# Kernel tuning notes

Measured on AMD Instinct MI355X. Metric: run time of the kernel, lower is better.

## Reference

```python
import jax, jax.numpy as jnp
import numpy as np

N_USERS = 90000
N_ITEMS = 60000
N = N_USERS + N_ITEMS   # 150000 total nodes
D = 64                  # emb_dim
K = 128                 # n_intents
E = 1600000             # directed edges
L = 3                   # n_layers
EPS = 1e-12


def setup_inputs() -> dict:
    key = jax.random.key(0)
    k0, k1, k2, k3, k4 = jax.random.split(key, 5)
    embeddings = jax.random.normal(k0, (N, D), dtype=jnp.float32) * 0.1
    user_intent = jax.random.normal(k1, (D, K), dtype=jnp.float32) * 0.1
    item_intent = jax.random.normal(k2, (D, K), dtype=jnp.float32) * 0.1
    all_h = jax.random.randint(k3, (E,), 0, N, dtype=jnp.int32)
    all_t = jax.random.randint(k4, (E,), 0, N, dtype=jnp.int32)
    return {"embeddings": embeddings, "user_intent": user_intent,
            "item_intent": item_intent, "all_h": all_h, "all_t": all_t}


def _spmm(vals, h, t, x):
    # y[i] = sum_{e: h[e]==i} vals[e] * x[t[e]]   (sparse adj @ x)
    return jax.ops.segment_sum(vals[:, None] * x[t], h, num_segments=N)


def _sym_norm_values(h, t):
    # G = D^{-1/2} A D^{-1/2} edge values (A has unit edge weights)
    deg = jax.ops.segment_sum(jnp.ones((E,), jnp.float32), h, num_segments=N)
    d_inv = jnp.where(deg > 0, deg ** -0.5, 0.0)
    return d_inv[h] * d_inv[t]


def _adaptive_values(head_emb, tail_emb, h):
    # F.normalize: x / max(||x||, eps)
    hn = head_emb / jnp.maximum(jnp.linalg.norm(head_emb, axis=1, keepdims=True), EPS)
    tn = tail_emb / jnp.maximum(jnp.linalg.norm(tail_emb, axis=1, keepdims=True), EPS)
    edge_alpha = (jnp.sum(hn * tn, axis=1) + 1.0) * 0.5          # [E]
    row_sum = jax.ops.segment_sum(edge_alpha, h, num_segments=N)  # degree scores
    d_inv = jnp.where(row_sum > 0, 1.0 / row_sum, 0.0)           # pow(-1).nan_to_num
    return d_inv[h] * edge_alpha


def reference(embeddings, user_intent, item_intent, all_h, all_t):
    g_vals = _sym_norm_values(all_h, all_t)
    x = embeddings
    acc = x  # sum over all layer embeddings (incl. layer 0)
    for _ in range(L):
        gnn = _spmm(g_vals, all_h, all_t, x)
        u, it = x[:N_USERS], x[N_USERS:]
        u_int = jax.nn.softmax(u @ user_intent, axis=1) @ user_intent.T
        i_int = jax.nn.softmax(it @ item_intent, axis=1) @ item_intent.T
        intl = jnp.concatenate([u_int, i_int], axis=0)            # [N, D]
        gaa_vals = _adaptive_values(gnn[all_h], gnn[all_t], all_h)
        iaa_vals = _adaptive_values(intl[all_h], intl[all_t], all_h)
        gaa = _spmm(gaa_vals, all_h, all_t, x)
        iaa = _spmm(iaa_vals, all_h, all_t, x)
        x = gnn + intl + gaa + iaa + x
        acc = acc + x
    return acc
```

## Files before the change

### kernel.cpp

```cpp
#include <hip/hip_runtime.h>

#define N_USERS 90000
#define N_ITEMS 60000
#define NN      (N_USERS + N_ITEMS)
#define D       64
#define KDIM    128
#define NE      1600000
#define EPSF    1e-12f
#define ROWD    64
#define TU      ((N_USERS + 63) / 64)
#define TI      ((N_ITEMS + 63) / 64)
#define NINT    (TU + TI)
#define RB      ((NN + 3) / 4)


typedef __fp16 h2 __attribute__((ext_vector_type(2)));
typedef float  f2 __attribute__((ext_vector_type(2)));

__device__ inline h2 as_h2(unsigned u) {
    union { unsigned u; h2 h; } v; v.u = u; return v.h;
}
__device__ inline unsigned pkrtz(float a, float b) {
    auto r = __builtin_amdgcn_cvt_pkrtz(a, b);
    union { decltype(r) h; unsigned u; } v; v.h = r; return v.u;
}
__device__ inline f2 dec8lo(unsigned u) {
    return __builtin_amdgcn_cvt_pk_f32_fp8((int)u, false);
}
__device__ inline f2 dec8hi(unsigned u) {
    return __builtin_amdgcn_cvt_pk_f32_fp8((int)u, true);
}
__device__ inline unsigned enc8(float a, float b, float c, float d) {
    int u = __builtin_amdgcn_cvt_pk_fp8_f32(a, b, 0, false);
    u = __builtin_amdgcn_cvt_pk_fp8_f32(c, d, u, true);
    return (unsigned)u;
}


#define EB   ((NE + 255) / 256)
#define IB   ((NN * 16 + 255) / 256)
#define PREG (EB + IB + 64)

__global__ void k_pre(const int* __restrict__ h, int* __restrict__ deg,
                      const float* __restrict__ emb,
                      float* __restrict__ acc, unsigned* __restrict__ pkA,
                      const float* __restrict__ Wu, const float* __restrict__ Wi,
                      float* __restrict__ WtG) {
    int bid = blockIdx.x;
    if (bid < EB) {
        int e = bid * 256 + threadIdx.x;
        if (e < NE) atomicAdd(&deg[h[e]], 1);
    } else if (bid < EB + IB) {
        int i = (bid - EB) * 256 + threadIdx.x;
        if (i >= NN * 16) return;
        float4 v = ((const float4*)emb)[i];
        ((float4*)acc)[i] = v;
        int row = i >> 4, l = i & 15;
        *(uint2*)&pkA[(size_t)row * ROWD + 32 + 2 * l] =
            make_uint2(pkrtz(v.x, v.y), pkrtz(v.z, v.w));
    } else {
        int i = (bid - EB - IB) * 256 + threadIdx.x;
        if (i >= 2 * D * KDIM) return;
        int m = i >> 13, r = i & 8191;
        int k = r >> 6, d = r & 63;
        const float* W = m ? Wi : Wu;
        WtG[m * 8192 + k * 64 + d] = W[d * KDIM + k];
    }
}

__global__ void k_rowoff(const int* __restrict__ deg, int* __restrict__ counter,
                         int* __restrict__ row_off, float* __restrict__ d_inv) {
    int i = blockIdx.x * blockDim.x + threadIdx.x;
    if (i >= NN) return;
    int d = deg[i];
    row_off[i] = atomicAdd(counter, d);
    d_inv[i]   = (d > 0) ? rsqrtf((float)d) : 0.f;
}

__global__ void k_scatter(const int* __restrict__ h, const int* __restrict__ t,
                          const int* __restrict__ row_off, int* __restrict__ row_cur,
                          const float* __restrict__ d_inv,
                          int2* __restrict__ csr) {
    int e = blockIdx.x * blockDim.x + threadIdx.x;
    if (e >= NE) return;
    int hh = h[e], tt = t[e];
    int slot = row_off[hh] + atomicAdd(&row_cur[hh], 1);
    csr[slot] = make_int2(tt, __float_as_int(d_inv[hh] * d_inv[tt]));
}

__global__ __launch_bounds__(256) void k_mid(const int* __restrict__ row_off,
                                             const int* __restrict__ deg,
                                             const int2* __restrict__ csr,
                                             unsigned* __restrict__ pk,
                                             unsigned* __restrict__ intl_h,
                                             const float* __restrict__ Wu,
                                             const float* __restrict__ Wi,
                                             const float* __restrict__ WtG,
                                             float* __restrict__ base_) {
    __shared__ float xs[64 * 68];
    int tid = threadIdx.x;
    int bid = blockIdx.x;

    if (bid < NINT) {
        unsigned* psU = (unsigned*)xs;
        const float* W;
        const float* Wt;
        int bse, count, n0;
        if (bid < TU) {
            W = Wu; Wt = WtG;        bse = 0;       count = N_USERS; n0 = bid * 64;
        } else {
            W = Wi; Wt = WtG + 8192; bse = N_USERS; count = N_ITEMS; n0 = (bid - TU) * 64;
        }

        for (int i = tid; i < 64 * 32; i += 256) {
            int nl = i >> 5, dw = i & 31;
            int n  = n0 + nl;
            unsigned u = (n < count) ? pk[(size_t)(bse + n) * ROWD + 32 + dw] : 0u;
            h2 xv = as_h2(u);
            xs[(2 * dw) * 68 + nl]     = (float)xv.x;
            xs[(2 * dw + 1) * 68 + nl] = (float)xv.y;
        }
        __syncthreads();

        int wv = tid >> 6;
        int la = tid & 63;
        int ag = la >> 4;
        int bg = la & 15;
        int nbase = wv * 16 + ag * 4;

        float acc[4][8];
        #pragma unroll
        for (int i = 0; i < 4; ++i)
            #pragma unroll
            for (int j = 0; j < 8; ++j) acc[i][j] = 0.f;

        #pragma unroll 4
        for (int d = 0; d < 64; ++d) {
            float4 xv = *(const float4*)&xs[d * 68 + nbase];
            float4 wa = *(const float4*)&W[d * KDIM + 4 * bg];
            float4 wb = *(const float4*)&W[d * KDIM + 64 + 4 * bg];
            float xx[4] = {xv.x, xv.y, xv.z, xv.w};
            float wk[8] = {wa.x, wa.y, wa.z, wa.w, wb.x, wb.y, wb.z, wb.w};
            #pragma unroll
            for (int i = 0; i < 4; ++i)
                #pragma unroll
                for (int j = 0; j < 8; ++j)
                    acc[i][j] = fmaf(xx[i], wk[j], acc[i][j]);
        }

        float p[4][8];
        float inv_s[4];
        #pragma unroll
        for (int i = 0; i < 4; ++i) {
            float m = acc[i][0];
            #pragma unroll
            for (int j = 1; j < 8; ++j) m = fmaxf(m, acc[i][j]);
            m = fmaxf(m, __shfl_xor(m, 1));
            m = fmaxf(m, __shfl_xor(m, 2));
            m = fmaxf(m, __shfl_xor(m, 4));
            m = fmaxf(m, __shfl_xor(m, 8));
            float sm = 0.f;
            #pragma unroll
            for (int j = 0; j < 8; ++j) { p[i][j] = __expf(acc[i][j] - m); sm += p[i][j]; }
            sm += __shfl_xor(sm, 1);
            sm += __shfl_xor(sm, 2);
            sm += __shfl_xor(sm, 4);
            sm += __shfl_xor(sm, 8);
            inv_s[i] = 1.f / sm;
        }

        __syncthreads();

        #pragma unroll
        for (int i = 0; i < 4; ++i) {
            float is = inv_s[i];
            #pragma unroll
            for (int j = 0; j < 2; ++j) {
                unsigned u0 = pkrtz(p[i][4 * j + 0] * is, p[i][4 * j + 1] * is);
                unsigned u1 = pkrtz(p[i][4 * j + 2] * is, p[i][4 * j + 3] * is);
                *(uint2*)&psU[(nbase + i) * 66 + 2 * bg + 32 * j] = make_uint2(u0, u1);
            }
        }
        __syncthreads();

        float o[4][4];
        #pragma unroll
        for (int i = 0; i < 4; ++i)
            #pragma unroll
            for (int r = 0; r < 4; ++r) o[i][r] = 0.f;

        int dbase = bg * 4;
        for (int kk = 0; kk < 32; ++kk) {
            uint2 P[4];
            #pragma unroll
            for (int i = 0; i < 4; ++i)
                P[i] = *(const uint2*)&psU[(nbase + i) * 66 + 2 * kk];
            float4 Wv[4];
            #pragma unroll
            for (int c = 0; c < 4; ++c)
                Wv[c] = *(const float4*)&Wt[(4 * kk + c) * 64 + dbase];
            #pragma unroll
            for (int i = 0; i < 4; ++i) {
                h2 pa = as_h2(P[i].x), pb = as_h2(P[i].y);
                float pc[4] = {(float)pa.x, (float)pa.y, (float)pb.x, (float)pb.y};
                #pragma unroll
                for (int c = 0; c < 4; ++c) {
                    o[i][0] = fmaf(pc[c], Wv[c].x, o[i][0]);
                    o[i][1] = fmaf(pc[c], Wv[c].y, o[i][1]);
                    o[i][2] = fmaf(pc[c], Wv[c].z, o[i][2]);
                    o[i][3] = fmaf(pc[c], Wv[c].w, o[i][3]);
                }
            }
        }

        #pragma unroll
        for (int i = 0; i < 4; ++i) {
            int n = n0 + nbase + i;
            float ss = o[i][0]*o[i][0] + o[i][1]*o[i][1] + o[i][2]*o[i][2] + o[i][3]*o[i][3];
            ss += __shfl_xor(ss, 1);
            ss += __shfl_xor(ss, 2);
            ss += __shfl_xor(ss, 4);
            ss += __shfl_xor(ss, 8);
            if (n < count) {
                size_t g = (size_t)(bse + n);
                float invn = 1.0f / fmaxf(sqrtf(ss), EPSF);
                *(uint2*)&intl_h[g * 32 + 2 * bg] =
                    make_uint2(pkrtz(o[i][0], o[i][1]), pkrtz(o[i][2], o[i][3]));
                pk[g * ROWD + 2 * bg + 1] =
                    enc8(o[i][0] * invn, o[i][1] * invn, o[i][2] * invn, o[i][3] * invn);
            }
        }
    } else {
        int wid  = (bid - NINT) * 4 + (tid >> 6);
        int lane = tid & 63;
        if (wid >= NN) return;
        int grp = lane >> 3, l8 = lane & 7;
        int s = row_off[wid], eend = s + deg[wid];
        float a0 = 0.f, a1 = 0.f, a2 = 0.f, a3 = 0.f;
        float a4 = 0.f, a5 = 0.f, a6 = 0.f, a7 = 0.f;
        int e = s;
        int2 c = csr[min(s + grp, eend - 1)];
        for (; e + 7 < eend; e += 8) {
            int2 cn = csr[min(e + 8 + grp, eend - 1)];
            uint4 w = *(const uint4*)&pk[(size_t)c.x * ROWD + 32 + 4 * l8];
            float gv = __int_as_float(c.y);
            h2 x0 = as_h2(w.x), x1 = as_h2(w.y), x2 = as_h2(w.z), x3 = as_h2(w.w);
            a0 = fmaf(gv, (float)x0.x, a0); a1 = fmaf(gv, (float)x0.y, a1);
            a2 = fmaf(gv, (float)x1.x, a2); a3 = fmaf(gv, (float)x1.y, a3);
            a4 = fmaf(gv, (float)x2.x, a4); a5 = fmaf(gv, (float)x2.y, a5);
            a6 = fmaf(gv, (float)x3.x, a6); a7 = fmaf(gv, (float)x3.y, a7);
            c = cn;
        }
        if (e < eend) {
            bool val = e + grp < eend;
            float gv = val ? __int_as_float(c.y) : 0.f;
            uint4 w = *(const uint4*)&pk[(size_t)c.x * ROWD + 32 + 4 * l8];
            h2 x0 = as_h2(w.x), x1 = as_h2(w.y), x2 = as_h2(w.z), x3 = as_h2(w.w);
            a0 = fmaf(gv, (float)x0.x, a0); a1 = fmaf(gv, (float)x0.y, a1);
            a2 = fmaf(gv, (float)x1.x, a2); a3 = fmaf(gv, (float)x1.y, a3);
            a4 = fmaf(gv, (float)x2.x, a4); a5 = fmaf(gv, (float)x2.y, a5);
            a6 = fmaf(gv, (float)x3.x, a6); a7 = fmaf(gv, (float)x3.y, a7);
        }
        #pragma unroll
        for (int m = 8; m <= 32; m <<= 1) {
            a0 += __shfl_xor(a0, m); a1 += __shfl_xor(a1, m);
            a2 += __shfl_xor(a2, m); a3 += __shfl_xor(a3, m);
            a4 += __shfl_xor(a4, m); a5 += __shfl_xor(a5, m);
            a6 += __shfl_xor(a6, m); a7 += __shfl_xor(a7, m);
        }
        float ss = fmaf(a0, a0, fmaf(a1, a1, fmaf(a2, a2, a3 * a3)))
                 + fmaf(a4, a4, fmaf(a5, a5, fmaf(a6, a6, a7 * a7)));
        ss += __shfl_xor(ss, 1); ss += __shfl_xor(ss, 2); ss += __shfl_xor(ss, 4);
        float inv = 1.f / fmaxf(sqrtf(ss), EPSF);
        if (grp == 0) {
            unsigned* pr = pk + (size_t)wid * ROWD;
            pr[4 * l8]     = enc8(a0 * inv, a1 * inv, a2 * inv, a3 * inv);
            pr[4 * l8 + 2] = enc8(a4 * inv, a5 * inv, a6 * inv, a7 * inv);
            uint4 xw = *(const uint4*)&pr[32 + 4 * l8];
            h2 x0 = as_h2(xw.x), x1 = as_h2(xw.y), x2 = as_h2(xw.z), x3 = as_h2(xw.w);
            float4* bp = (float4*)base_ + (size_t)wid * 16 + 2 * l8;
            bp[0] = make_float4(a0 + (float)x0.x, a1 + (float)x0.y,
                                a2 + (float)x1.x, a3 + (float)x1.y);
            bp[1] = make_float4(a4 + (float)x2.x, a5 + (float)x2.y,
                                a6 + (float)x3.x, a7 + (float)x3.y);
        }
    }
}

__global__ __launch_bounds__(256) void k_fused(const int* __restrict__ row_off,
                                               const int* __restrict__ deg,
                                               const int2* __restrict__ csr,
                                               const unsigned* __restrict__ pk,
                                               const unsigned* __restrict__ intl_h,
                                               const float* __restrict__ base_,
                                               unsigned* __restrict__ pknext,
                                               float* __restrict__ acc) {
    int wid  = (blockIdx.x * blockDim.x + threadIdx.x) >> 6;
    int lane = threadIdx.x & 63;
    if (wid >= NN) return;
    int grp = lane >> 4, l16 = lane & 15;

    const unsigned* ph = pk + (size_t)wid * ROWD;
    uint2 hq = *(const uint2*)&ph[2 * l16];
    f2 hgl = dec8lo(hq.x), hgh = dec8hi(hq.x);
    f2 hil = dec8lo(hq.y), hih = dec8hi(hq.y);

    int s = row_off[wid], eend = s + deg[wid];
    float sg = 0.f, si = 0.f;
    float g0 = 0.f, g1 = 0.f, g2 = 0.f, g3 = 0.f;
    float i0 = 0.f, i1 = 0.f, i2 = 0.f, i3 = 0.f;

    int e = s;
    int tA = csr[min(s + grp, eend - 1)].x;
    int tB = csr[min(s + 4 + grp, eend - 1)].x;
    for (; e + 7 < eend; e += 8) {
        int tA2 = csr[min(e + 8 + grp, eend - 1)].x;
        int tB2 = csr[min(e + 12 + grp, eend - 1)].x;
        const unsigned* pA = pk + (size_t)tA * ROWD;
        const unsigned* pB = pk + (size_t)tB * ROWD;
        uint2 qA = *(const uint2*)&pA[2 * l16];
        uint2 wA = *(const uint2*)&pA[32 + 2 * l16];
        uint2 qB = *(const uint2*)&pB[2 * l16];
        uint2 wB = *(const uint2*)&pB[32 + 2 * l16];
        f2 gA01 = dec8lo(qA.x), gA23 = dec8hi(qA.x);
        f2 iA01 = dec8lo(qA.y), iA23 = dec8hi(qA.y);
        f2 gB01 = dec8lo(qB.x), gB23 = dec8hi(qB.x);
        f2 iB01 = dec8lo(qB.y), iB23 = dec8hi(qB.y);
        float pgA = fmaf(hgl.x, gA01.x, fmaf(hgl.y, gA01.y,
                    fmaf(hgh.x, gA23.x, hgh.y * gA23.y)));
        float piA = fmaf(hil.x, iA01.x, fmaf(hil.y, iA01.y,
                    fmaf(hih.x, iA23.x, hih.y * iA23.y)));
        float pgB = fmaf(hgl.x, gB01.x, fmaf(hgl.y, gB01.y,
                    fmaf(hgh.x, gB23.x, hgh.y * gB23.y)));
        float piB = fmaf(hil.x, iB01.x, fmaf(hil.y, iB01.y,
                    fmaf(hih.x, iB23.x, hih.y * iB23.y)));
        #pragma unroll
        for (int m = 1; m <= 8; m <<= 1) {
            pgA += __shfl_xor(pgA, m); piA += __shfl_xor(piA, m);
            pgB += __shfl_xor(pgB, m); piB += __shfl_xor(piB, m);
        }
        float agA = fmaf(pgA, 0.5f, 0.5f), aiA = fmaf(piA, 0.5f, 0.5f);
        float agB = fmaf(pgB, 0.5f, 0.5f), aiB = fmaf(piB, 0.5f, 0.5f);
        sg += agA + agB; si += aiA + aiB;
        h2 xa0 = as_h2(wA.x), xa1 = as_h2(wA.y);
        h2 xb0 = as_h2(wB.x), xb1 = as_h2(wB.y);
        g0 = fmaf(agA, (float)xa0.x, g0); g1 = fmaf(agA, (float)xa0.y, g1);
        g2 = fmaf(agA, (float)xa1.x, g2); g3 = fmaf(agA, (float)xa1.y, g3);
        i0 = fmaf(aiA, (float)xa0.x, i0); i1 = fmaf(aiA, (float)xa0.y, i1);
        i2 = fmaf(aiA, (float)xa1.x, i2); i3 = fmaf(aiA, (float)xa1.y, i3);
        g0 = fmaf(agB, (float)xb0.x, g0); g1 = fmaf(agB, (float)xb0.y, g1);
        g2 = fmaf(agB, (float)xb1.x, g2); g3 = fmaf(agB, (float)xb1.y, g3);
        i0 = fmaf(aiB, (float)xb0.x, i0); i1 = fmaf(aiB, (float)xb0.y, i1);
        i2 = fmaf(aiB, (float)xb1.x, i2); i3 = fmaf(aiB, (float)xb1.y, i3);
        tA = tA2; tB = tB2;
    }
    #pragma unroll
    for (int r = 0; r < 2; ++r) {
        if (e >= eend) break;
        int t = (r == 0) ? tA : tB;
        bool val = e + grp < eend;
        const unsigned* pr = pk + (size_t)t * ROWD;
        uint2 q = *(const uint2*)&pr[2 * l16];
        uint2 w = *(const uint2*)&pr[32 + 2 * l16];
        f2 tg01 = dec8lo(q.x), tg23 = dec8hi(q.x);
        f2 ti01 = dec8lo(q.y), ti23 = dec8hi(q.y);
        float pg = fmaf(hgl.x, tg01.x, fmaf(hgl.y, tg01.y,
                   fmaf(hgh.x, tg23.x, hgh.y * tg23.y)));
        float pi = fmaf(hil.x, ti01.x, fmaf(hil.y, ti01.y,
                   fmaf(hih.x, ti23.x, hih.y * ti23.y)));
        #pragma unroll
        for (int m = 1; m <= 8; m <<= 1) {
            pg += __shfl_xor(pg, m); pi += __shfl_xor(pi, m);
        }
        float ag = fmaf(pg, 0.5f, 0.5f), ai = fmaf(pi, 0.5f, 0.5f);
        if (!val) { ag = 0.f; ai = 0.f; }
        sg += ag; si += ai;
        h2 x0 = as_h2(w.x), x1 = as_h2(w.y);
        g0 = fmaf(ag, (float)x0.x, g0); g1 = fmaf(ag, (float)x0.y, g1);
        g2 = fmaf(ag, (float)x1.x, g2); g3 = fmaf(ag, (float)x1.y, g3);
        i0 = fmaf(ai, (float)x0.x, i0); i1 = fmaf(ai, (float)x0.y, i1);
        i2 = fmaf(ai, (float)x1.x, i2); i3 = fmaf(ai, (float)x1.y, i3);
        e += 4;
    }

    #pragma unroll
    for (int m = 16; m <= 32; m <<= 1) {
        sg += __shfl_xor(sg, m); si += __shfl_xor(si, m);
        g0 += __shfl_xor(g0, m); g1 += __shfl_xor(g1, m);
        g2 += __shfl_xor(g2, m); g3 += __shfl_xor(g3, m);
        i0 += __shfl_xor(i0, m); i1 += __shfl_xor(i1, m);
        i2 += __shfl_xor(i2, m); i3 += __shfl_xor(i3, m);
    }

    if (grp == 0) {
        float invg = sg > 0.f ? 1.f / sg : 0.f;
        float invi = si > 0.f ? 1.f / si : 0.f;
        size_t bidx = (size_t)wid * 16 + l16;
        float4 b = ((const float4*)base_)[bidx];
        uint2 iw = *(const uint2*)&intl_h[(size_t)wid * 32 + 2 * l16];
        h2 il0 = as_h2(iw.x), il1 = as_h2(iw.y);
        float o0 = b.x + (float)il0.x + invg * g0 + invi * i0;
        float o1 = b.y + (float)il0.y + invg * g1 + invi * i1;
        float o2 = b.z + (float)il1.x + invg * g2 + invi * i2;
        float o3 = b.w + (float)il1.y + invg * g3 + invi * i3;
        *(uint2*)&pknext[(size_t)wid * ROWD + 32 + 2 * l16] =
            make_uint2(pkrtz(o0, o1), pkrtz(o2, o3));
        float4 a = ((float4*)acc)[bidx];
        a.x += o0; a.y += o1; a.z += o2; a.w += o3;
        ((float4*)acc)[bidx] = a;
    }
}


extern "C" void kernel_launch(void* const* d_in, const int* in_sizes, int n_in,
                              void* d_out, int out_size, void* d_ws, size_t ws_size,
                              hipStream_t stream) {
    const float* emb   = (const float*)d_in[0];
    const float* Wu    = (const float*)d_in[1];
    const float* Wi    = (const float*)d_in[2];
    const int*   all_h = (const int*)d_in[3];
    const int*   all_t = (const int*)d_in[4];
    float*       acc   = (float*)d_out;

    char*  bp  = (char*)d_ws;
    size_t off = 0;
    auto take = [&](size_t bytes) -> char* {
        char* r = bp + off;
        off = (off + bytes + 255) & ~(size_t)255;
        return r;
    };
    int*      deg     = (int*)     take((size_t)NN * 4);
    int*      row_off = (int*)     take((size_t)NN * 4);
    int*      row_cur = (int*)     take((size_t)NN * 4);
    int*      counter = (int*)     take(256);
    float*    d_inv   = (float*)   take((size_t)NN * 4);
    int2*     csr     = (int2*)    take((size_t)NE * 8);
    unsigned* pkA     = (unsigned*)take((size_t)NN * ROWD * 4);
    unsigned* pkB     = (unsigned*)take((size_t)NN * ROWD * 4);
    unsigned* intl_h  = (unsigned*)take((size_t)NN * 32 * 4);
    float*    base_   = (float*)   take((size_t)NN * D * 4);
    float*    WtG     = (float*)   take((size_t)2 * D * KDIM * 4);
    (void)ws_size; (void)in_sizes; (void)n_in; (void)out_size;

    hipMemsetAsync(deg, 0, (size_t)NN * 4, stream);
    hipMemsetAsync(row_cur, 0, (size_t)NN * 4, stream);
    hipMemsetAsync(counter, 0, 256, stream);

    const int NBK = (NN + 255) / 256;
    k_pre<<<PREG, 256, 0, stream>>>(all_h, deg, emb, acc, pkA, Wu, Wi, WtG);
    k_rowoff<<<NBK, 256, 0, stream>>>(deg, counter, row_off, d_inv);
    k_scatter<<<EB, 256, 0, stream>>>(all_h, all_t, row_off, row_cur, d_inv, csr);

    unsigned* cur = pkA;
    unsigned* nxt = pkB;
    for (int l = 0; l < 3; ++l) {
        k_mid<<<NINT + RB, 256, 0, stream>>>(row_off, deg, csr, cur, intl_h,
                                             Wu, Wi, WtG, base_);
        k_fused<<<RB, 256, 0, stream>>>(row_off, deg, csr, cur, intl_h,
                                        base_, nxt, acc);
        unsigned* tmp = cur; cur = nxt; nxt = tmp;
    }
}
```

Before: 910.3 us.

## Compute intent softmax matmuls with fp16 MFMA and pre-packed weight fragments

Replaces the scalar FMA loops for the two intent matmuls (x@W and softmax@W^T) in k_mid with 16x16x32 fp16 MFMA instructions. The weights are pre-packed once in k_pre into per-lane fragment layouts, and the softmax probabilities pass through swizzled LDS to feed the second MFMA. This removes the LDS transpose staging and the fp32 FMA work. In exchange, the weights and probabilities now go through fp16 inputs, and the output write uses lane shuffles and partially masked stores.

New measurement: 792.0 us. -13.0%, faster.

```diff
diff --git a/kernel.cpp b/kernel.cpp
--- a/kernel.cpp
+++ b/kernel.cpp
@@ -15,10 +15,15 @@
 
 
 typedef __fp16 h2 __attribute__((ext_vector_type(2)));
+typedef __fp16 h8 __attribute__((ext_vector_type(8)));
 typedef float  f2 __attribute__((ext_vector_type(2)));
+typedef float  f4v __attribute__((ext_vector_type(4)));
 
 __device__ inline h2 as_h2(unsigned u) {
     union { unsigned u; h2 h; } v; v.u = u; return v.h;
+}
+__device__ inline h8 as_h8(uint4 u) {
+    union { uint4 u; h8 h; } v; v.u = u; return v.h;
 }
 __device__ inline unsigned pkrtz(float a, float b) {
     auto r = __builtin_amdgcn_cvt_pkrtz(a, b);
@@ -39,13 +44,13 @@
 
 #define EB   ((NE + 255) / 256)
 #define IB   ((NN * 16 + 255) / 256)
-#define PREG (EB + IB + 64)
+#define PREG (EB + IB + 16)
 
 __global__ void k_pre(const int* __restrict__ h, int* __restrict__ deg,
                       const float* __restrict__ emb,
                       float* __restrict__ acc, unsigned* __restrict__ pkA,
                       const float* __restrict__ Wu, const float* __restrict__ Wi,
-                      float* __restrict__ WtG) {
+                      uint4* __restrict__ WfA, uint4* __restrict__ Wf2) {
     int bid = blockIdx.x;
     if (bid < EB) {
         int e = bid * 256 + threadIdx.x;
@@ -60,11 +65,28 @@
             make_uint2(pkrtz(v.x, v.y), pkrtz(v.z, v.w));
     } else {
         int i = (bid - EB - IB) * 256 + threadIdx.x;
-        if (i >= 2 * D * KDIM) return;
-        int m = i >> 13, r = i & 8191;
-        int k = r >> 6, d = r & 63;
-        const float* W = m ? Wi : Wu;
-        WtG[m * 8192 + k * 64 + d] = W[d * KDIM + k];
+        if (i >= 4096) return;
+        int ph  = i >> 11;
+        int r   = i & 2047;
+        int mat = r >> 10;
+        int rr  = r & 1023;
+        const float* W = mat ? Wi : Wu;
+        union { __fp16 hh[8]; uint4 u; } pkt;
+        if (!ph) {
+            int nt = rr >> 7, ks = (rr >> 6) & 1, lane = rr & 63;
+            int q = lane >> 4, c = lane & 15;
+            #pragma unroll
+            for (int j = 0; j < 8; ++j)
+                pkt.hh[j] = (__fp16)W[(32 * ks + 8 * q + j) * KDIM + nt * 16 + c];
+            WfA[((mat * 8 + nt) * 2 + ks) * 64 + lane] = pkt.u;
+        } else {
+            int nt = rr >> 8, ks = (rr >> 6) & 3, lane = rr & 63;
+            int q = lane >> 4, c = lane & 15;
+            #pragma unroll
+            for (int j = 0; j < 8; ++j)
+                pkt.hh[j] = (__fp16)W[(nt * 16 + c) * KDIM + 32 * ks + 8 * q + j];
+            Wf2[((mat * 4 + nt) * 4 + ks) * 64 + lane] = pkt.u;
+        }
     }
 }
 
@@ -93,141 +115,115 @@
                                              const int2* __restrict__ csr,
                                              unsigned* __restrict__ pk,
                                              unsigned* __restrict__ intl_h,
-                                             const float* __restrict__ Wu,
-                                             const float* __restrict__ Wi,
-                                             const float* __restrict__ WtG,
+                                             const uint4* __restrict__ WfA,
+                                             const uint4* __restrict__ Wf2,
                                              float* __restrict__ base_) {
-    __shared__ float xs[64 * 68];
+    __shared__ unsigned Plds[4096];
     int tid = threadIdx.x;
     int bid = blockIdx.x;
 
     if (bid < NINT) {
-        unsigned* psU = (unsigned*)xs;
-        const float* W;
-        const float* Wt;
-        int bse, count, n0;
-        if (bid < TU) {
-            W = Wu; Wt = WtG;        bse = 0;       count = N_USERS; n0 = bid * 64;
-        } else {
-            W = Wi; Wt = WtG + 8192; bse = N_USERS; count = N_ITEMS; n0 = (bid - TU) * 64;
-        }
-
-        for (int i = tid; i < 64 * 32; i += 256) {
-            int nl = i >> 5, dw = i & 31;
-            int n  = n0 + nl;
-            unsigned u = (n < count) ? pk[(size_t)(bse + n) * ROWD + 32 + dw] : 0u;
-            h2 xv = as_h2(u);
-            xs[(2 * dw) * 68 + nl]     = (float)xv.x;
-            xs[(2 * dw + 1) * 68 + nl] = (float)xv.y;
-        }
-        __syncthreads();
-
-        int wv = tid >> 6;
-        int la = tid & 63;
-        int ag = la >> 4;
-        int bg = la & 15;
-        int nbase = wv * 16 + ag * 4;
-
-        float acc[4][8];
-        #pragma unroll
-        for (int i = 0; i < 4; ++i)
-            #pragma unroll
-            for (int j = 0; j < 8; ++j) acc[i][j] = 0.f;
-
-        #pragma unroll 4
-        for (int d = 0; d < 64; ++d) {
-            float4 xv = *(const float4*)&xs[d * 68 + nbase];
-            float4 wa = *(const float4*)&W[d * KDIM + 4 * bg];
-            float4 wb = *(const float4*)&W[d * KDIM + 64 + 4 * bg];
-            float xx[4] = {xv.x, xv.y, xv.z, xv.w};
-            float wk[8] = {wa.x, wa.y, wa.z, wa.w, wb.x, wb.y, wb.z, wb.w};
-            #pragma unroll
-            for (int i = 0; i < 4; ++i)
-                #pragma unroll
-                for (int j = 0; j < 8; ++j)
-                    acc[i][j] = fmaf(xx[i], wk[j], acc[i][j]);
-        }
-
-        float p[4][8];
+        int mat, bse, count, n0;
+        if (bid < TU) { mat = 0; bse = 0;       count = N_USERS; n0 = bid * 64; }
+        else          { mat = 1; bse = N_USERS; count = N_ITEMS; n0 = (bid - TU) * 64; }
+
+        int wv = tid >> 6, la = tid & 63;
+        int q = la >> 4, c = la & 15;
+
+        int nA = n0 + wv * 16 + c;
+        size_t gA = (size_t)min(bse + nA, NN - 1);
+        const unsigned* prA = pk + gA * ROWD;
+        uint4 a0u = *(const uint4*)&prA[32 + 4 * q];
+        uint4 a1u = *(const uint4*)&prA[48 + 4 * q];
+
+        f4v S[8];
+        #pragma unroll
+        for (int nt = 0; nt < 8; ++nt) S[nt] = (f4v){0.f, 0.f, 0.f, 0.f};
+        const uint4* WA = WfA + (size_t)mat * 1024;
+        #pragma unroll
+        for (int nt = 0; nt < 8; ++nt) {
+            h8 B0 = as_h8(WA[(nt * 2 + 0) * 64 + la]);
+            h8 B1 = as_h8(WA[(nt * 2 + 1) * 64 + la]);
+            S[nt] = __builtin_amdgcn_mfma_f32_16x16x32_f16(as_h8(a0u), B0, S[nt], 0, 0, 0);
+            S[nt] = __builtin_amdgcn_mfma_f32_16x16x32_f16(as_h8(a1u), B1, S[nt], 0, 0, 0);
+        }
+
         float inv_s[4];
         #pragma unroll
-        for (int i = 0; i < 4; ++i) {
-            float m = acc[i][0];
-            #pragma unroll
-            for (int j = 1; j < 8; ++j) m = fmaxf(m, acc[i][j]);
-            m = fmaxf(m, __shfl_xor(m, 1));
-            m = fmaxf(m, __shfl_xor(m, 2));
-            m = fmaxf(m, __shfl_xor(m, 4));
-            m = fmaxf(m, __shfl_xor(m, 8));
+        for (int reg = 0; reg < 4; ++reg) {
+            float m = S[0][reg];
+            #pragma unroll
+            for (int nt = 1; nt < 8; ++nt) m = fmaxf(m, S[nt][reg]);
+            m = fmaxf(m, __shfl_xor(m, 1)); m = fmaxf(m, __shfl_xor(m, 2));
+            m = fmaxf(m, __shfl_xor(m, 4)); m = fmaxf(m, __shfl_xor(m, 8));
             float sm = 0.f;
             #pragma unroll
-            for (int j = 0; j < 8; ++j) { p[i][j] = __expf(acc[i][j] - m); sm += p[i][j]; }
-            sm += __shfl_xor(sm, 1);
-            sm += __shfl_xor(sm, 2);
-            sm += __shfl_xor(sm, 4);
-            sm += __shfl_xor(sm, 8);
-            inv_s[i] = 1.f / sm;
-        }
-
-        __syncthreads();
-
-        #pragma unroll
-        for (int i = 0; i < 4; ++i) {
-            float is = inv_s[i];
-            #pragma unroll
-            for (int j = 0; j < 2; ++j) {
-                unsigned u0 = pkrtz(p[i][4 * j + 0] * is, p[i][4 * j + 1] * is);
-                unsigned u1 = pkrtz(p[i][4 * j + 2] * is, p[i][4 * j + 3] * is);
-                *(uint2*)&psU[(nbase + i) * 66 + 2 * bg + 32 * j] = make_uint2(u0, u1);
+            for (int nt = 0; nt < 8; ++nt) {
+                float e_ = __expf(S[nt][reg] - m);
+                S[nt][reg] = e_;
+                sm += e_;
             }
-        }
-        __syncthreads();
-
-        float o[4][4];
-        #pragma unroll
-        for (int i = 0; i < 4; ++i)
-            #pragma unroll
-            for (int r = 0; r < 4; ++r) o[i][r] = 0.f;
-
-        int dbase = bg * 4;
-        for (int kk = 0; kk < 32; ++kk) {
-            uint2 P[4];
-            #pragma unroll
-            for (int i = 0; i < 4; ++i)
-                P[i] = *(const uint2*)&psU[(nbase + i) * 66 + 2 * kk];
-            float4 Wv[4];
-            #pragma unroll
-            for (int c = 0; c < 4; ++c)
-                Wv[c] = *(const float4*)&Wt[(4 * kk + c) * 64 + dbase];
-            #pragma unroll
-            for (int i = 0; i < 4; ++i) {
-                h2 pa = as_h2(P[i].x), pb = as_h2(P[i].y);
-                float pc[4] = {(float)pa.x, (float)pa.y, (float)pb.x, (float)pb.y};
-                #pragma unroll
-                for (int c = 0; c < 4; ++c) {
-                    o[i][0] = fmaf(pc[c], Wv[c].x, o[i][0]);
-                    o[i][1] = fmaf(pc[c], Wv[c].y, o[i][1]);
-                    o[i][2] = fmaf(pc[c], Wv[c].z, o[i][2]);
-                    o[i][3] = fmaf(pc[c], Wv[c].w, o[i][3]);
+            sm += __shfl_xor(sm, 1); sm += __shfl_xor(sm, 2);
+            sm += __shfl_xor(sm, 4); sm += __shfl_xor(sm, 8);
+            inv_s[reg] = 1.f / sm;
+        }
+
+        #pragma unroll
+        for (int reg = 0; reg < 4; ++reg) {
+            int ln = wv * 16 + q * 4 + reg;
+            #pragma unroll
+            for (int nt = 0; nt < 8; ++nt) {
+                float v  = S[nt][reg] * inv_s[reg];
+                float v1 = __shfl_xor(v, 1);
+                if (!(c & 1)) {
+                    int byte_in_row = nt * 32 + c * 2;
+                    int sw = byte_in_row ^ ((ln & 7) << 4);
+                    *(unsigned*)((char*)Plds + ln * 256 + sw) = pkrtz(v, v1);
                 }
             }
         }
 
-        #pragma unroll
-        for (int i = 0; i < 4; ++i) {
-            int n = n0 + nbase + i;
-            float ss = o[i][0]*o[i][0] + o[i][1]*o[i][1] + o[i][2]*o[i][2] + o[i][3]*o[i][3];
-            ss += __shfl_xor(ss, 1);
-            ss += __shfl_xor(ss, 2);
-            ss += __shfl_xor(ss, 4);
-            ss += __shfl_xor(ss, 8);
-            if (n < count) {
-                size_t g = (size_t)(bse + n);
-                float invn = 1.0f / fmaxf(sqrtf(ss), EPSF);
-                *(uint2*)&intl_h[g * 32 + 2 * bg] =
-                    make_uint2(pkrtz(o[i][0], o[i][1]), pkrtz(o[i][2], o[i][3]));
-                pk[g * ROWD + 2 * bg + 1] =
-                    enc8(o[i][0] * invn, o[i][1] * invn, o[i][2] * invn, o[i][3] * invn);
+        f4v O[4];
+        #pragma unroll
+        for (int nt = 0; nt < 4; ++nt) O[nt] = (f4v){0.f, 0.f, 0.f, 0.f};
+        const uint4* W2 = Wf2 + (size_t)mat * 1024;
+        int lnA = wv * 16 + c;
+        #pragma unroll
+        for (int ks = 0; ks < 4; ++ks) {
+            int byte_in_row = (32 * ks + 8 * q) * 2;
+            int sw = byte_in_row ^ ((lnA & 7) << 4);
+            uint4 au = *(const uint4*)((char*)Plds + lnA * 256 + sw);
+            #pragma unroll
+            for (int nt = 0; nt < 4; ++nt) {
+                h8 Bp = as_h8(W2[(nt * 4 + ks) * 64 + la]);
+                O[nt] = __builtin_amdgcn_mfma_f32_16x16x32_f16(as_h8(au), Bp, O[nt], 0, 0, 0);
+            }
+        }
+
+        #pragma unroll
+        for (int reg = 0; reg < 4; ++reg) {
+            float ss = 0.f;
+            #pragma unroll
+            for (int nt = 0; nt < 4; ++nt) ss = fmaf(O[nt][reg], O[nt][reg], ss);
+            ss += __shfl_xor(ss, 1); ss += __shfl_xor(ss, 2);
+            ss += __shfl_xor(ss, 4); ss += __shfl_xor(ss, 8);
+            float invn = 1.f / fmaxf(sqrtf(ss), EPSF);
+            int n = n0 + wv * 16 + q * 4 + reg;
+            bool valid = n < count;
+            size_t g = (size_t)(bse + n);
+            #pragma unroll
+            for (int nt = 0; nt < 4; ++nt) {
+                float v  = O[nt][reg];
+                float v1 = __shfl_xor(v, 1);
+                float v2 = __shfl_xor(v, 2);
+                float v3 = __shfl_xor(v, 3);
+                if (valid) {
+                    if (!(c & 1))
+                        intl_h[g * 32 + ((nt * 16 + c) >> 1)] = pkrtz(v, v1);
+                    if (!(c & 3))
+                        pk[g * ROWD + 2 * ((nt * 16 + c) >> 2) + 1] =
+                            enc8(v * invn, v1 * invn, v2 * invn, v3 * invn);
+                }
             }
         }
     } else {
@@ -439,7 +435,8 @@
     unsigned* pkB     = (unsigned*)take((size_t)NN * ROWD * 4);
     unsigned* intl_h  = (unsigned*)take((size_t)NN * 32 * 4);
     float*    base_   = (float*)   take((size_t)NN * D * 4);
-    float*    WtG     = (float*)   take((size_t)2 * D * KDIM * 4);
+    uint4*    WfA     = (uint4*)   take((size_t)2048 * 16);
+    uint4*    Wf2     = (uint4*)   take((size_t)2048 * 16);
     (void)ws_size; (void)in_sizes; (void)n_in; (void)out_size;
 
     hipMemsetAsync(deg, 0, (size_t)NN * 4, stream);
@@ -447,7 +444,7 @@
     hipMemsetAsync(counter, 0, 256, stream);
 
     const int NBK = (NN + 255) / 256;
-    k_pre<<<PREG, 256, 0, stream>>>(all_h, deg, emb, acc, pkA, Wu, Wi, WtG);
+    k_pre<<<PREG, 256, 0, stream>>>(all_h, deg, emb, acc, pkA, Wu, Wi, WfA, Wf2);
     k_rowoff<<<NBK, 256, 0, stream>>>(deg, counter, row_off, d_inv);
     k_scatter<<<EB, 256, 0, stream>>>(all_h, all_t, row_off, row_cur, d_inv, csr);
 
@@ -455,7 +452,7 @@
     unsigned* nxt = pkB;
     for (int l = 0; l < 3; ++l) {
         k_mid<<<NINT + RB, 256, 0, stream>>>(row_off, deg, csr, cur, intl_h,
-                                             Wu, Wi, WtG, base_);
+                                             WfA, Wf2, base_);
         k_fused<<<RB, 256, 0, stream>>>(row_off, deg, csr, cur, intl_h,
                                         base_, nxt, acc);
         unsigned* tmp = cur; cur = nxt; nxt = tmp;
```
